# Kernel optimization log

Hardware: AMD Instinct MI355X
Metric: run time of the kernel (lower is better)

The kernel has to match this reference:

```python
import jax, jax.numpy as jnp
import numpy as np

D_MODEL = 1024
N_HEAD = 16
DK = D_MODEL // N_HEAD
D_FF = 2048
EPS = 1e-6
NEG = -1e10


def layer_norm(x, gamma, beta):
    # torch .std() is unbiased (N-1), and eps is added to std (not var)
    mean = jnp.mean(x, axis=-1, keepdims=True)
    var = jnp.sum((x - mean) ** 2, axis=-1, keepdims=True) / (x.shape[-1] - 1)
    std = jnp.sqrt(var)
    return gamma * (x - mean) / (std + EPS) + beta


def setup_inputs() -> dict:
    key = jax.random.key(0)
    ks = jax.random.split(key, 12)
    s = 0.02
    inp = {
        'x': jax.random.normal(ks[0], (16, 512, D_MODEL), dtype=jnp.float32),
        'x_mask': jax.random.randint(ks[1], (16, 1, 1, 512), 0, 2, dtype=jnp.int32),
        'Wq': jax.random.normal(ks[2], (D_MODEL, D_MODEL), dtype=jnp.float32) * s,
        'bq': jnp.zeros((D_MODEL,), jnp.float32),
        'Wk': jax.random.normal(ks[3], (D_MODEL, D_MODEL), dtype=jnp.float32) * s,
        'bk': jnp.zeros((D_MODEL,), jnp.float32),
        'Wv': jax.random.normal(ks[4], (D_MODEL, D_MODEL), dtype=jnp.float32) * s,
        'bv': jnp.zeros((D_MODEL,), jnp.float32),
        'Wo': jax.random.normal(ks[5], (D_MODEL, D_MODEL), dtype=jnp.float32) * s,
        'bo': jnp.zeros((D_MODEL,), jnp.float32),
        'gamma1': jnp.ones((D_MODEL,), jnp.float32),
        'beta1': jnp.zeros((D_MODEL,), jnp.float32),
        'W1': jax.random.normal(ks[6], (D_MODEL, D_FF), dtype=jnp.float32) * s,
        'b1': jnp.zeros((D_FF,), jnp.float32),
        'W2': jax.random.normal(ks[7], (D_FF, D_MODEL), dtype=jnp.float32) * s,
        'b2': jnp.zeros((D_MODEL,), jnp.float32),
        'gamma2': jnp.ones((D_MODEL,), jnp.float32),
        'beta2': jnp.zeros((D_MODEL,), jnp.float32),
    }
    return inp


def reference(x, x_mask, Wq, bq, Wk, bk, Wv, bv, Wo, bo, gamma1, beta1,
              W1, b1, W2, b2, gamma2, beta2):
    B, S, _ = x.shape
    # QKV projections -> [B, S, H, DK]
    q = (x @ Wq + bq).reshape(B, S, N_HEAD, DK)
    k = (x @ Wk + bk).reshape(B, S, N_HEAD, DK)
    v = (x @ Wv + bv).reshape(B, S, N_HEAD, DK)
    # scores [B, H, Sq, Sk]
    scores = jnp.einsum('bqhd,bkhd->bhqk', q, k) / jnp.sqrt(jnp.float32(DK))
    scores = jnp.where(x_mask == 0, jnp.float32(NEG), scores)
    probs = jax.nn.softmax(scores, axis=-1)
    attn = jnp.einsum('bhqk,bkhd->bqhd', probs, v).reshape(B, S, D_MODEL)
    attn_out = attn @ Wo + bo
    # residual + post-LN 1
    h = layer_norm(attn_out + x, gamma1, beta1)
    # FFN (exact GELU as torch nn.GELU default)
    ffn = jax.nn.gelu(h @ W1 + b1, approximate=False) @ W2 + b2
    out = layer_norm(ffn + h, gamma2, beta2)
    return out
```

## Files before the change

kernel.cpp:

```cpp
#include <hip/hip_runtime.h>
#include <math.h>

#define B_ 16
#define S_ 512
#define DM 1024
#define NH 16
#define DFF 2048

typedef short bf16x8 __attribute__((ext_vector_type(8)));
typedef float f32x4 __attribute__((ext_vector_type(4)));
typedef unsigned short u16;

__device__ __forceinline__ u16 f2bf(float f) {
  unsigned int u = __float_as_uint(f);
  u += 0x7FFF + ((u >> 16) & 1);
  return (u16)(u >> 16);
}

__device__ __forceinline__ float bf2f(u16 u) {
  return __uint_as_float(((unsigned)u) << 16);
}

__device__ __forceinline__ unsigned cvtpk_bf16(float lo, float hi) {
  unsigned r;
  asm("v_cvt_pk_bf16_f32 %0, %1, %2" : "=v"(r) : "v"(lo), "v"(hi));
  return r;
}

__device__ __forceinline__ float gelu_exact(float x) {
  return 0.5f * x * (1.0f + erff(x * 0.70710678118654752f));
}

__device__ __forceinline__ void gload_lds16(const void* g, void* l) {
  __builtin_amdgcn_global_load_lds((const __attribute__((address_space(1))) void*)g,
                                   (__attribute__((address_space(3))) void*)l, 16, 0, 0);
}

#define QSCALE 0.18033688011112042f
#define MASKNEG -1.442695e10f


__global__ void cvt_bf16_k(const float* __restrict__ in, u16* __restrict__ out, int n) {
  int i = (blockIdx.x * blockDim.x + threadIdx.x) * 4;
  float4 v = *(const float4*)(in + i);
  uint2 pk;
  pk.x = (unsigned)f2bf(v.x) | ((unsigned)f2bf(v.y) << 16);
  pk.y = (unsigned)f2bf(v.z) | ((unsigned)f2bf(v.w) << 16);
  *(uint2*)(out + i) = pk;
}

__global__ __launch_bounds__(256)
void prep_weights(const float* __restrict__ Wq, const float* __restrict__ Wk,
                  const float* __restrict__ Wv, const float* __restrict__ Wo,
                  const float* __restrict__ W1, const float* __restrict__ W2,
                  u16* __restrict__ wqkvt, u16* __restrict__ wot,
                  u16* __restrict__ w1t, u16* __restrict__ w2t,
                  const float* __restrict__ bq, const float* __restrict__ bk,
                  const float* __restrict__ bv, float* __restrict__ bqkv) {
  const int bid = blockIdx.x;
  if (bid >= 8192) {
    int i = (bid - 8192) * 256 + threadIdx.x;
    bqkv[i] = (i < 1024) ? bq[i] : ((i < 2048) ? bk[i - 1024] : bv[i - 2048]);
    return;
  }
  const float* W;
  u16* Wt;
  int K, N, bx, by;
  if (bid < 4096) {
    const int m = bid >> 10, t = bid & 1023;
    K = 1024; N = 1024; bx = t & 31; by = t >> 5;
    W = (m == 0) ? Wq : (m == 1) ? Wk : (m == 2) ? Wv : Wo;
    Wt = (m == 3) ? wot : wqkvt + m * 1048576;
  } else if (bid < 6144) {
    const int t = bid - 4096;
    K = 1024; N = 2048; bx = t & 63; by = t >> 6; W = W1; Wt = w1t;
  } else {
    const int t = bid - 6144;
    K = 2048; N = 1024; bx = t & 31; by = t >> 5; W = W2; Wt = w2t;
  }
  __shared__ float tile[32][33];
  const int n0 = bx * 32, k0 = by * 32;
  const int tx = threadIdx.x & 31, ty = threadIdx.x >> 5;
#pragma unroll
  for (int j = 0; j < 32; j += 8)
    tile[ty + j][tx] = W[(size_t)(k0 + ty + j) * N + n0 + tx];
  __syncthreads();
#pragma unroll
  for (int j = 0; j < 32; j += 8)
    Wt[(size_t)(n0 + ty + j) * K + k0 + tx] = f2bf(tile[tx][ty + j]);
}

template <int EPI>
__global__ __launch_bounds__(256, 2)
void gemm_mfma(const u16* __restrict__ A, const u16* __restrict__ Bt,
               const float* __restrict__ bias, void* __restrict__ Cout,
               u16* __restrict__ vT, int M, int N, int K) {
  __shared__ __align__(16) char lds[73728];
  const int tid = threadIdx.x;
  const int w = tid >> 6, lane = tid & 63;
  const int wm = w >> 1, wn = w & 1;

  const int gx = gridDim.x;
  const int nwg = gx * gridDim.y;
  const int lin = blockIdx.y * gx + blockIdx.x;
  const int wg = (lin & 7) * (nwg >> 3) + (lin >> 3);
  const int bm = wg / gx, bn = wg % gx;

  const int NT = K >> 5;

  const int srow = w * 16 + (lane >> 2);
  const int skel = ((lane & 3) ^ (lane >> 4)) * 8;
  const u16* gA = A + (size_t)(bm * 256 + srow) * K + skel;
  const u16* gB = Bt + (size_t)(bn * 128 + srow) * K + skel;
  const size_t rs64 = (size_t)64 * K;
  const int dstb = w * 1024;

  const int lr = lane & 15, kg = lane >> 4;
  const int kslot = (kg ^ ((lr >> 2) & 3)) << 4;
  const int fAoff = (wm * 128 + lr) * 64 + kslot;
  const int fBoff = 16384 + (wn * 64 + lr) * 64 + kslot;

  f32x4 acc[8][4];
#pragma unroll
  for (int i = 0; i < 8; ++i)
#pragma unroll
    for (int j = 0; j < 4; ++j) acc[i][j] = (f32x4){0.f, 0.f, 0.f, 0.f};

#define STAGE_A(t_, sl_)                                         \
  do {                                                           \
    const u16* g_ = gA + (size_t)(t_) * 32;                      \
    char* d_ = lds + (sl_) * 24576 + dstb;                       \
    gload_lds16(g_, d_);                                         \
    gload_lds16(g_ + rs64, d_ + 4096);                           \
    gload_lds16(g_ + 2 * rs64, d_ + 8192);                       \
    gload_lds16(g_ + 3 * rs64, d_ + 12288);                      \
  } while (0)
#define STAGE_B(t_, sl_)                                         \
  do {                                                           \
    const u16* g_ = gB + (size_t)(t_) * 32;                      \
    char* d_ = lds + (sl_) * 24576 + 16384 + dstb;               \
    gload_lds16(g_, d_);                                         \
    gload_lds16(g_ + rs64, d_ + 4096);                           \
  } while (0)

  STAGE_A(0, 0);
  STAGE_B(0, 0);
  STAGE_A(1, 1);
  STAGE_B(1, 1);
  asm volatile("s_waitcnt vmcnt(6)" ::: "memory");
  __builtin_amdgcn_s_barrier();
  __builtin_amdgcn_sched_barrier(0);

  int cs = 0, ss = 2;
  for (int t = 0; t < NT; ++t) {
    const int st = (t + 2 < NT) ? (t + 2) : (NT - 1);
    const char* fA = lds + cs * 24576 + fAoff;
    const char* fB = lds + cs * 24576 + fBoff;
    bf16x8 av[4], bv[4];
#pragma unroll
    for (int mi = 0; mi < 4; ++mi) av[mi] = *(const bf16x8*)(fA + mi * 1024);
#pragma unroll
    for (int ni = 0; ni < 4; ++ni) bv[ni] = *(const bf16x8*)(fB + ni * 1024);
    STAGE_A(st, ss);
    __builtin_amdgcn_s_setprio(1);
#pragma unroll
    for (int mi = 0; mi < 4; ++mi)
#pragma unroll
      for (int ni = 0; ni < 4; ++ni)
        acc[mi][ni] = __builtin_amdgcn_mfma_f32_16x16x32_bf16(av[mi], bv[ni], acc[mi][ni], 0, 0, 0);
    __builtin_amdgcn_s_setprio(0);
    bf16x8 av2[4];
#pragma unroll
    for (int mi = 0; mi < 4; ++mi) av2[mi] = *(const bf16x8*)(fA + 4096 + mi * 1024);
    STAGE_B(st, ss);
    __builtin_amdgcn_s_setprio(1);
#pragma unroll
    for (int mi = 0; mi < 4; ++mi)
#pragma unroll
      for (int ni = 0; ni < 4; ++ni)
        acc[4 + mi][ni] = __builtin_amdgcn_mfma_f32_16x16x32_bf16(av2[mi], bv[ni], acc[4 + mi][ni], 0, 0, 0);
    __builtin_amdgcn_s_setprio(0);
    asm volatile("s_waitcnt vmcnt(6) lgkmcnt(0)" ::: "memory");
    __builtin_amdgcn_s_barrier();
    __builtin_amdgcn_sched_barrier(0);
    cs = (cs == 2) ? 0 : cs + 1;
    ss = (ss == 2) ? 0 : ss + 1;
  }
#undef STAGE_A
#undef STAGE_B

  const int crow0 = bm * 256 + wm * 128;
  const int ccol0 = bn * 128 + wn * 64;
#pragma unroll
  for (int mi = 0; mi < 8; ++mi) {
#pragma unroll
    for (int ni = 0; ni < 4; ++ni) {
      const int col = ccol0 + ni * 16 + lr;
      const float bv_ = bias[col];
      const int rowb = crow0 + mi * 16 + (lane >> 4) * 4;
      float v[4];
#pragma unroll
      for (int r = 0; r < 4; ++r) v[r] = acc[mi][ni][r] + bv_;
      if (EPI == 1) {
#pragma unroll
        for (int r = 0; r < 4; ++r)
          ((u16*)Cout)[(size_t)(rowb + r) * N + col] = f2bf(gelu_exact(v[r]));
      } else if (EPI == 2) {
#pragma unroll
        for (int r = 0; r < 4; ++r)
          ((float*)Cout)[(size_t)(rowb + r) * N + col] = v[r];
      } else if (EPI == 4) {
#pragma unroll
        for (int r = 0; r < 4; ++r)
          ((u16*)Cout)[(size_t)(rowb + r) * N + col] = f2bf(v[r]);
      } else {
        if (col < 2048) {
          const float sc = (col < 1024) ? QSCALE : 1.0f;
#pragma unroll
          for (int r = 0; r < 4; ++r)
            ((u16*)Cout)[(size_t)(rowb + r) * 2048 + col] = f2bf(v[r] * sc);
        } else {
          const int b = rowb >> 9, s = rowb & 511;
          const int hd = col - 2048;
          ushort4 pk;
          pk.x = f2bf(v[0]); pk.y = f2bf(v[1]); pk.z = f2bf(v[2]); pk.w = f2bf(v[3]);
          *(ushort4*)(vT + ((size_t)(b * NH + (hd >> 6)) * 64 + (hd & 63)) * S_ + s) = pk;
        }
      }
    }
  }
}

__global__ __launch_bounds__(256, 3)
void attn_kernel(const u16* __restrict__ qk,
                 const u16* __restrict__ vT,
                 const int* __restrict__ mask,
                 u16* __restrict__ out) {
  __shared__ __align__(16) u16 Qs[32 * 72];
  __shared__ __align__(16) u16 Pl[32 * 520];
  __shared__ __align__(16) float Mlf[512];
  __shared__ __align__(16) float Rsum[32][4];

  const int tid = threadIdx.x;
  const int w = tid >> 6, lane = tid & 63;
  const int bid = blockIdx.x;
  const int widx = (bid & 7) * 512 + (bid >> 3);
  const int qt = widx & 15, h = (widx >> 4) & 15, b = widx >> 8;
  const int q0 = qt * 32;
  const int arow = lane & 15, kg = lane >> 4;

  {
    int r = tid >> 3, slot = tid & 7;
    bf16x8 v = *(const bf16x8*)(qk + (size_t)(b * S_ + q0 + r) * 2048 + h * 64 + slot * 8);
    *(bf16x8*)((char*)Qs + r * 144 + slot * 16) = v;
  }
  Mlf[tid] = (mask[b * S_ + tid] == 0) ? MASKNEG : 0.f;
  Mlf[tid + 256] = (mask[b * S_ + tid + 256] == 0) ? MASKNEG : 0.f;

  const u16* vb = vT + ((size_t)(b * NH + h) * 64 + w * 16 + arow) * S_ + kg * 8;
  bf16x8 vv[8];
#pragma unroll
  for (int i = 0; i < 8; ++i) vv[i] = *(const bf16x8*)(vb + i * 32);

  __syncthreads();

  bf16x8 qf[2][2];
#pragma unroll
  for (int mi = 0; mi < 2; ++mi)
#pragma unroll
    for (int kk = 0; kk < 2; ++kk)
      qf[mi][kk] = *(const bf16x8*)((char*)Qs + (mi * 16 + arow) * 144 + kk * 64 + kg * 16);

  f32x4 s0[8], s1[8];
  const u16* kbase = qk + (size_t)(b * S_) * 2048 + 1024 + h * 64 + kg * 8;
#pragma unroll
  for (int half = 0; half < 2; ++half) {
    bf16x8 kvl[4][2];
#pragma unroll
    for (int j = 0; j < 4; ++j) {
      const int colg = w * 128 + (half * 4 + j) * 16 + arow;
      const u16* kr = kbase + (size_t)colg * 2048;
      kvl[j][0] = *(const bf16x8*)(kr);
      kvl[j][1] = *(const bf16x8*)(kr + 32);
    }
#pragma unroll
    for (int j = 0; j < 4; ++j) {
      const int ni = half * 4 + j;
      f32x4 a0 = {0.f, 0.f, 0.f, 0.f}, a1 = {0.f, 0.f, 0.f, 0.f};
      a0 = __builtin_amdgcn_mfma_f32_16x16x32_bf16(kvl[j][0], qf[0][0], a0, 0, 0, 0);
      a0 = __builtin_amdgcn_mfma_f32_16x16x32_bf16(kvl[j][1], qf[0][1], a0, 0, 0, 0);
      a1 = __builtin_amdgcn_mfma_f32_16x16x32_bf16(kvl[j][0], qf[1][0], a1, 0, 0, 0);
      a1 = __builtin_amdgcn_mfma_f32_16x16x32_bf16(kvl[j][1], qf[1][1], a1, 0, 0, 0);
      const f32x4 mb = *(const f32x4*)&Mlf[w * 128 + ni * 16 + kg * 4];
      s0[ni] = a0 + mb;
      s1[ni] = a1 + mb;
    }
  }

  f32x4 ac0 = {0.f, 0.f, 0.f, 0.f}, ac1 = ac0;
#pragma unroll
  for (int ni = 0; ni < 8; ++ni) {
#pragma unroll
    for (int r = 0; r < 4; ++r) {
      s0[ni][r] = __builtin_amdgcn_exp2f(s0[ni][r]);
      s1[ni][r] = __builtin_amdgcn_exp2f(s1[ni][r]);
    }
    ac0 += s0[ni];
    ac1 += s1[ni];
  }
  float t0 = ac0[0] + ac0[1] + ac0[2] + ac0[3];
  float t1 = ac1[0] + ac1[1] + ac1[2] + ac1[3];
  t0 += __shfl_xor(t0, 16);
  t0 += __shfl_xor(t0, 32);
  t1 += __shfl_xor(t1, 16);
  t1 += __shfl_xor(t1, 32);
  if (kg == 0) {
    Rsum[arow][w] = t0;
    Rsum[16 + arow][w] = t1;
  }

  {
    const int kq = w * 128 + kg * 4;
    char* const p0 = (char*)Pl + (arow * 520 + kq) * 2;
    char* const p1 = (char*)Pl + ((16 + arow) * 520 + kq) * 2;
#pragma unroll
    for (int ni = 0; ni < 8; ++ni) {
      uint2 pk;
      pk.x = cvtpk_bf16(s0[ni][0], s0[ni][1]);
      pk.y = cvtpk_bf16(s0[ni][2], s0[ni][3]);
      *(uint2*)(p0 + ni * 32) = pk;
      pk.x = cvtpk_bf16(s1[ni][0], s1[ni][1]);
      pk.y = cvtpk_bf16(s1[ni][2], s1[ni][3]);
      *(uint2*)(p1 + ni * 32) = pk;
    }
  }
  __syncthreads();

  {
    f32x4 oa[2];
    oa[0] = (f32x4){0.f, 0.f, 0.f, 0.f};
    oa[1] = (f32x4){0.f, 0.f, 0.f, 0.f};
#pragma unroll
    for (int t16 = 0; t16 < 16; ++t16) {
      const int sk0 = t16 * 32;
      bf16x8 bfr = (t16 < 8) ? vv[t16] : *(const bf16x8*)(vb + t16 * 32);
#pragma unroll
      for (int mi = 0; mi < 2; ++mi) {
        bf16x8 pa = *(const bf16x8*)(Pl + (mi * 16 + arow) * 520 + sk0 + kg * 8);
        oa[mi] = __builtin_amdgcn_mfma_f32_16x16x32_bf16(pa, bfr, oa[mi], 0, 0, 0);
      }
    }
#pragma unroll
    for (int mi = 0; mi < 2; ++mi)
#pragma unroll
      for (int r = 0; r < 4; ++r) {
        const int rloc = mi * 16 + kg * 4 + r;
        f32x4 sv = *(const f32x4*)&Rsum[rloc][0];
        const float inv = 1.0f / (sv[0] + sv[1] + sv[2] + sv[3]);
        const int qrow = q0 + rloc;
        out[(size_t)(b * S_ + qrow) * DM + h * 64 + w * 16 + arow] = f2bf(oa[mi][r] * inv);
      }
  }
}

template <int AB, int RB, int WF, int WB>
__global__ __launch_bounds__(256)
void ln_kernel(const void* __restrict__ a, const void* __restrict__ res,
               const float* __restrict__ gamma, const float* __restrict__ beta,
               float* __restrict__ outf, u16* __restrict__ outb) {
  const int row = blockIdx.x, tid = threadIdx.x;
  const int w = tid >> 6, lane = tid & 63;
  const size_t base = (size_t)row * DM + tid * 4;
  float v0, v1, v2, v3;
  {
    float a0, a1, a2, a3, r0, r1, r2, r3;
    if (AB) {
      ushort4 u = *(const ushort4*)((const u16*)a + base);
      a0 = bf2f(u.x); a1 = bf2f(u.y); a2 = bf2f(u.z); a3 = bf2f(u.w);
    } else {
      float4 u = *(const float4*)((const float*)a + base);
      a0 = u.x; a1 = u.y; a2 = u.z; a3 = u.w;
    }
    if (RB) {
      ushort4 u = *(const ushort4*)((const u16*)res + base);
      r0 = bf2f(u.x); r1 = bf2f(u.y); r2 = bf2f(u.z); r3 = bf2f(u.w);
    } else {
      float4 u = *(const float4*)((const float*)res + base);
      r0 = u.x; r1 = u.y; r2 = u.z; r3 = u.w;
    }
    v0 = a0 + r0; v1 = a1 + r1; v2 = a2 + r2; v3 = a3 + r3;
  }
  float s = v0 + v1 + v2 + v3;
  float ss = v0 * v0 + v1 * v1 + v2 * v2 + v3 * v3;
#pragma unroll
  for (int off = 32; off >= 1; off >>= 1) {
    s += __shfl_down(s, off);
    ss += __shfl_down(ss, off);
  }
  __shared__ float ps[4], pss[4], mb[2];
  if (lane == 0) { ps[w] = s; pss[w] = ss; }
  __syncthreads();
  if (tid == 0) {
    float S = ps[0] + ps[1] + ps[2] + ps[3];
    float SS = pss[0] + pss[1] + pss[2] + pss[3];
    float mean = S * (1.0f / DM);
    float var = (SS - (float)DM * mean * mean) * (1.0f / (DM - 1));
    var = fmaxf(var, 0.f);
    mb[0] = mean;
    mb[1] = 1.0f / (sqrtf(var) + 1e-6f);
  }
  __syncthreads();
  const float mean = mb[0], rinv = mb[1];
  const int c = tid * 4;
  float y0 = gamma[c] * (v0 - mean) * rinv + beta[c];
  float y1 = gamma[c + 1] * (v1 - mean) * rinv + beta[c + 1];
  float y2 = gamma[c + 2] * (v2 - mean) * rinv + beta[c + 2];
  float y3 = gamma[c + 3] * (v3 - mean) * rinv + beta[c + 3];
  if (WF) {
    float4 o = {y0, y1, y2, y3};
    *(float4*)(outf + base) = o;
  }
  if (WB) {
    uint2 pk;
    pk.x = (unsigned)f2bf(y0) | ((unsigned)f2bf(y1) << 16);
    pk.y = (unsigned)f2bf(y2) | ((unsigned)f2bf(y3) << 16);
    *(uint2*)(outb + base) = pk;
  }
}


extern "C" void kernel_launch(void* const* d_in, const int* in_sizes, int n_in,
                              void* d_out, int out_size, void* d_ws, size_t ws_size,
                              hipStream_t stream) {
  const float* x = (const float*)d_in[0];
  const int* xm = (const int*)d_in[1];
  const float* Wq = (const float*)d_in[2];
  const float* bq = (const float*)d_in[3];
  const float* Wk = (const float*)d_in[4];
  const float* bk = (const float*)d_in[5];
  const float* Wv = (const float*)d_in[6];
  const float* bv = (const float*)d_in[7];
  const float* Wo = (const float*)d_in[8];
  const float* bo = (const float*)d_in[9];
  const float* g1 = (const float*)d_in[10];
  const float* be1 = (const float*)d_in[11];
  const float* W1 = (const float*)d_in[12];
  const float* b1 = (const float*)d_in[13];
  const float* W2 = (const float*)d_in[14];
  const float* b2 = (const float*)d_in[15];
  const float* g2 = (const float*)d_in[16];
  const float* be2 = (const float*)d_in[17];

  char* ws = (char*)d_ws;
  u16* xb = (u16*)(ws);
  u16* wqkvt = (u16*)(ws + 16777216);
  u16* wot = (u16*)(ws + 23068672);
  u16* w1t = (u16*)(ws + 25165824);
  u16* w2t = (u16*)(ws + 29360128);
  float* bqkv = (float*)(ws + 33554432);
  u16* qkb = (u16*)(ws + 33566720);
  u16* vtb = (u16*)(ws + 67121152);
  u16* attnb = (u16*)(ws + 83898368);
  u16* attnpb = (u16*)(ws + 100675584);
  u16* f2b = (u16*)(ws + 117452800);
  u16* hb = xb;

  cvt_bf16_k<<<dim3(8192), dim3(256), 0, stream>>>(x, xb, 8388608);
  prep_weights<<<dim3(8204), dim3(256), 0, stream>>>(Wq, Wk, Wv, Wo, W1, W2,
                                                     wqkvt, wot, w1t, w2t,
                                                     bq, bk, bv, bqkv);

  gemm_mfma<3><<<dim3(24, 32), dim3(256), 0, stream>>>(xb, wqkvt, bqkv, (void*)qkb, vtb, 8192, 3072, 1024);
  attn_kernel<<<dim3(4096), dim3(256), 0, stream>>>(qkb, vtb, xm, attnb);
  gemm_mfma<4><<<dim3(8, 32), dim3(256), 0, stream>>>(attnb, wot, bo, (void*)attnpb, (u16*)nullptr, 8192, 1024, 1024);
  ln_kernel<1, 0, 0, 1><<<dim3(8192), dim3(256), 0, stream>>>(attnpb, x, g1, be1, (float*)nullptr, hb);
  gemm_mfma<1><<<dim3(16, 32), dim3(256), 0, stream>>>(hb, w1t, b1, (void*)qkb, (u16*)nullptr, 8192, 2048, 1024);
  gemm_mfma<4><<<dim3(8, 32), dim3(256), 0, stream>>>(qkb, w2t, b2, (void*)f2b, (u16*)nullptr, 8192, 1024, 2048);
  ln_kernel<1, 1, 1, 0><<<dim3(8192), dim3(256), 0, stream>>>(f2b, hb, g2, be2, (float*)d_out, (u16*)nullptr);
}
```

Baseline: 291.7 us.

## Process two query tiles per attention block with 512 threads

The attention kernel now launches 2048 blocks of 512 threads, each handling 64 query rows as two 32-row halves that share one head and batch. The mask bias array is loaded once per block and shared by both halves, and launch bounds move from (256,3) to (512,4). The intent is to cut per-block setup cost and to let the two halves hit the same K/V data in cache together. The cost is doubled LDS per block and a tighter register budget under the new launch bounds, which could lower occupancy or cause spills.

```diff
diff --git a/kernel.cpp b/kernel.cpp
--- a/kernel.cpp
+++ b/kernel.cpp
@@ -231,33 +231,33 @@
   }
 }
 
-__global__ __launch_bounds__(256, 3)
+__global__ __launch_bounds__(512, 4)
 void attn_kernel(const u16* __restrict__ qk,
                  const u16* __restrict__ vT,
                  const int* __restrict__ mask,
                  u16* __restrict__ out) {
-  __shared__ __align__(16) u16 Qs[32 * 72];
-  __shared__ __align__(16) u16 Pl[32 * 520];
+  __shared__ __align__(16) u16 Qs[2][32 * 72];
+  __shared__ __align__(16) u16 Pl[2][32 * 520];
   __shared__ __align__(16) float Mlf[512];
-  __shared__ __align__(16) float Rsum[32][4];
+  __shared__ __align__(16) float Rsum[2][32][4];
 
   const int tid = threadIdx.x;
   const int w = tid >> 6, lane = tid & 63;
+  const int wl = w & 3, qsel = w >> 2;
   const int bid = blockIdx.x;
-  const int widx = (bid & 7) * 512 + (bid >> 3);
-  const int qt = widx & 15, h = (widx >> 4) & 15, b = widx >> 8;
-  const int q0 = qt * 32;
+  const int widx = (bid & 7) * 256 + (bid >> 3);
+  const int qt8 = widx & 7, h = (widx >> 3) & 15, b = widx >> 7;
+  const int q0 = qt8 * 64 + qsel * 32;
   const int arow = lane & 15, kg = lane >> 4;
 
   {
     int r = tid >> 3, slot = tid & 7;
-    bf16x8 v = *(const bf16x8*)(qk + (size_t)(b * S_ + q0 + r) * 2048 + h * 64 + slot * 8);
-    *(bf16x8*)((char*)Qs + r * 144 + slot * 16) = v;
+    bf16x8 v = *(const bf16x8*)(qk + (size_t)(b * S_ + qt8 * 64 + r) * 2048 + h * 64 + slot * 8);
+    *(bf16x8*)((char*)Qs[r >> 5] + (r & 31) * 144 + slot * 16) = v;
   }
   Mlf[tid] = (mask[b * S_ + tid] == 0) ? MASKNEG : 0.f;
-  Mlf[tid + 256] = (mask[b * S_ + tid + 256] == 0) ? MASKNEG : 0.f;
-
-  const u16* vb = vT + ((size_t)(b * NH + h) * 64 + w * 16 + arow) * S_ + kg * 8;
+
+  const u16* vb = vT + ((size_t)(b * NH + h) * 64 + wl * 16 + arow) * S_ + kg * 8;
   bf16x8 vv[8];
 #pragma unroll
   for (int i = 0; i < 8; ++i) vv[i] = *(const bf16x8*)(vb + i * 32);
@@ -269,7 +269,7 @@
   for (int mi = 0; mi < 2; ++mi)
 #pragma unroll
     for (int kk = 0; kk < 2; ++kk)
-      qf[mi][kk] = *(const bf16x8*)((char*)Qs + (mi * 16 + arow) * 144 + kk * 64 + kg * 16);
+      qf[mi][kk] = *(const bf16x8*)((char*)Qs[qsel] + (mi * 16 + arow) * 144 + kk * 64 + kg * 16);
 
   f32x4 s0[8], s1[8];
   const u16* kbase = qk + (size_t)(b * S_) * 2048 + 1024 + h * 64 + kg * 8;
@@ -278,7 +278,7 @@
     bf16x8 kvl[4][2];
 #pragma unroll
     for (int j = 0; j < 4; ++j) {
-      const int colg = w * 128 + (half * 4 + j) * 16 + arow;
+      const int colg = wl * 128 + (half * 4 + j) * 16 + arow;
       const u16* kr = kbase + (size_t)colg * 2048;
       kvl[j][0] = *(const bf16x8*)(kr);
       kvl[j][1] = *(const bf16x8*)(kr + 32);
@@ -291,7 +291,7 @@
       a0 = __builtin_amdgcn_mfma_f32_16x16x32_bf16(kvl[j][1], qf[0][1], a0, 0, 0, 0);
       a1 = __builtin_amdgcn_mfma_f32_16x16x32_bf16(kvl[j][0], qf[1][0], a1, 0, 0, 0);
       a1 = __builtin_amdgcn_mfma_f32_16x16x32_bf16(kvl[j][1], qf[1][1], a1, 0, 0, 0);
-      const f32x4 mb = *(const f32x4*)&Mlf[w * 128 + ni * 16 + kg * 4];
+      const f32x4 mb = *(const f32x4*)&Mlf[wl * 128 + ni * 16 + kg * 4];
       s0[ni] = a0 + mb;
       s1[ni] = a1 + mb;
     }
@@ -315,14 +315,14 @@
   t1 += __shfl_xor(t1, 16);
   t1 += __shfl_xor(t1, 32);
   if (kg == 0) {
-    Rsum[arow][w] = t0;
-    Rsum[16 + arow][w] = t1;
+    Rsum[qsel][arow][wl] = t0;
+    Rsum[qsel][16 + arow][wl] = t1;
   }
 
   {
-    const int kq = w * 128 + kg * 4;
-    char* const p0 = (char*)Pl + (arow * 520 + kq) * 2;
-    char* const p1 = (char*)Pl + ((16 + arow) * 520 + kq) * 2;
+    const int kq = wl * 128 + kg * 4;
+    char* const p0 = (char*)Pl[qsel] + (arow * 520 + kq) * 2;
+    char* const p1 = (char*)Pl[qsel] + ((16 + arow) * 520 + kq) * 2;
 #pragma unroll
     for (int ni = 0; ni < 8; ++ni) {
       uint2 pk;
@@ -346,7 +346,7 @@
       bf16x8 bfr = (t16 < 8) ? vv[t16] : *(const bf16x8*)(vb + t16 * 32);
 #pragma unroll
       for (int mi = 0; mi < 2; ++mi) {
-        bf16x8 pa = *(const bf16x8*)(Pl + (mi * 16 + arow) * 520 + sk0 + kg * 8);
+        bf16x8 pa = *(const bf16x8*)(Pl[qsel] + (mi * 16 + arow) * 520 + sk0 + kg * 8);
         oa[mi] = __builtin_amdgcn_mfma_f32_16x16x32_bf16(pa, bfr, oa[mi], 0, 0, 0);
       }
     }
@@ -355,10 +355,10 @@
 #pragma unroll
       for (int r = 0; r < 4; ++r) {
         const int rloc = mi * 16 + kg * 4 + r;
-        f32x4 sv = *(const f32x4*)&Rsum[rloc][0];
+        f32x4 sv = *(const f32x4*)&Rsum[qsel][rloc][0];
         const float inv = 1.0f / (sv[0] + sv[1] + sv[2] + sv[3]);
         const int qrow = q0 + rloc;
-        out[(size_t)(b * S_ + qrow) * DM + h * 64 + w * 16 + arow] = f2bf(oa[mi][r] * inv);
+        out[(size_t)(b * S_ + qrow) * DM + h * 64 + wl * 16 + arow] = f2bf(oa[mi][r] * inv);
       }
   }
 }
@@ -471,7 +471,7 @@
                                                      bq, bk, bv, bqkv);
 
   gemm_mfma<3><<<dim3(24, 32), dim3(256), 0, stream>>>(xb, wqkvt, bqkv, (void*)qkb, vtb, 8192, 3072, 1024);
-  attn_kernel<<<dim3(4096), dim3(256), 0, stream>>>(qkb, vtb, xm, attnb);
+  attn_kernel<<<dim3(2048), dim3(512), 0, stream>>>(qkb, vtb, xm, attnb);
   gemm_mfma<4><<<dim3(8, 32), dim3(256), 0, stream>>>(attnb, wot, bo, (void*)attnpb, (u16*)nullptr, 8192, 1024, 1024);
   ln_kernel<1, 0, 0, 1><<<dim3(8192), dim3(256), 0, stream>>>(attnpb, x, g1, be1, (float*)nullptr, hb);
   gemm_mfma<1><<<dim3(16, 32), dim3(256), 0, stream>>>(hb, w1t, b1, (void*)qkb, (u16*)nullptr, 8192, 2048, 1024);
```

Measured after the change: 295.6 us. Within noise of the previous version (+1.3%).
